# Kernel optimization log

Measured on AMD Instinct MI355X. Metric: run time of the kernel, lower is better.

## Reference

```python
import jax, jax.numpy as jnp
import numpy as np

DIM = 128
HEADS = 128
DV = DIM // HEADS  # 1 (scalar attention values per head)
TOPK = 32
CHUNK = 16384
DEPTH = 2
STATE = 262144
BLOCK = 256
NBLOCKS = STATE // BLOCK
HIDDEN = int(DIM * 8 / 3)  # 341, SwiGLU hidden
EPS = float(jnp.finfo(jnp.float32).eps)  # torch RMSNorm default eps


def rmsnorm(x, w):
    return x * jax.lax.rsqrt(jnp.mean(x * x, axis=-1, keepdims=True) + EPS) * w


def swiglu(x, w_gate, w_up, w_down):
    return (jax.nn.silu(x @ w_gate.T) * (x @ w_up.T)) @ w_down.T


def topk_attention(x, Wq, Wk, Wv, Wo):
    b, n, d = x.shape
    q = jnp.einsum('bnd,hd->bhn', x, Wq)      # (b,h,n) scalar queries
    keys = jnp.einsum('bnd,hd->bhn', x, Wk)   # (b,h,n) scalar keys
    v = (x @ Wv.T).reshape(b, n, HEADS, DV).transpose(0, 2, 1, 3)  # (b,h,n,dv)
    order = jnp.argsort(keys, axis=-1)
    k_sorted = jnp.take_along_axis(keys, order, axis=-1)
    v_sorted = jnp.take_along_axis(v, order[..., None], axis=2)
    top_k_keys = k_sorted[..., -TOPK:]
    bot_k_keys = k_sorted[..., :TOPK]
    top_k_vals = v_sorted[:, :, -TOPK:, :]
    bot_k_vals = v_sorted[:, :, :TOPK, :]
    nc = n // CHUNK
    q_chunks = q.reshape(b, HEADS, nc, CHUNK).transpose(2, 0, 1, 3)  # (nc,b,h,c)

    def chunk_fn(q_chunk):
        scores_top = q_chunk[..., None] * top_k_keys[:, :, None, :]  # (b,h,c,k)
        scores_bot = q_chunk[..., None] * bot_k_keys[:, :, None, :]
        attn_top = jax.nn.softmax(scores_top, axis=-1)
        attn_bot = jax.nn.softmax(scores_bot, axis=-1)
        out_top = jnp.einsum('bhck,bhkd->bhcd', attn_top, top_k_vals)
        out_bot = jnp.einsum('bhck,bhkd->bhcd', attn_bot, bot_k_vals)
        q_pos = (q_chunk > 0).astype(x.dtype)[..., None]
        return q_pos * out_top + (1 - q_pos) * out_bot  # (b,h,c,dv)

    out = jax.lax.map(chunk_fn, q_chunks)            # (nc,b,h,c,dv)
    out = out.transpose(1, 0, 3, 2, 4).reshape(b, n, d)  # (b,n,h*dv)
    return out @ Wo.T


def setup_inputs() -> dict:
    key = jax.random.key(0)
    ks = jax.random.split(key, 16)
    s = 0.02
    nrm = lambda k, shp: (jax.random.normal(k, shp, dtype=jnp.float32) * s)
    inp = {}
    inp['state_bytes'] = jax.random.randint(ks[0], (1, STATE), 0, 256)
    inp['byte_embed'] = nrm(ks[1], (256, DIM))
    inp['block_pos_embed'] = nrm(ks[2], (NBLOCKS, DIM))
    inp['local_pos_embed'] = nrm(ks[3], (BLOCK, DIM))
    inp['Wq'] = nrm(ks[4], (DEPTH, HEADS, DIM))
    inp['Wk'] = nrm(ks[5], (DEPTH, HEADS, DIM))
    inp['Wv'] = nrm(ks[6], (DEPTH, DIM, DIM))
    inp['Wo'] = nrm(ks[7], (DEPTH, DIM, DIM))
    inp['norm1_w'] = jnp.ones((DEPTH, DIM), dtype=jnp.float32)
    inp['norm2_w'] = jnp.ones((DEPTH, DIM), dtype=jnp.float32)
    inp['w_gate'] = nrm(ks[8], (DEPTH, HIDDEN, DIM))
    inp['w_up'] = nrm(ks[9], (DEPTH, HIDDEN, DIM))
    inp['w_down'] = nrm(ks[10], (DEPTH, DIM, HIDDEN))
    inp['final_norm_w'] = jnp.ones((DIM,), dtype=jnp.float32)
    inp['out_w'] = nrm(ks[11], (256, DIM))
    return inp


def reference(state_bytes, byte_embed, block_pos_embed, local_pos_embed, Wq, Wk, Wv, Wo,
              norm1_w, norm2_w, w_gate, w_up, w_down, final_norm_w, out_w):
    x = byte_embed[state_bytes]                                   # (b,n,d)
    block_pos = jnp.repeat(block_pos_embed, BLOCK, axis=0)        # (n,d)
    local_pos = jnp.tile(local_pos_embed, (NBLOCKS, 1))           # (n,d)
    x = x + block_pos[None] + local_pos[None]
    for l in range(DEPTH):
        x = x + topk_attention(rmsnorm(x, norm1_w[l]), Wq[l], Wk[l], Wv[l], Wo[l])
        x = x + swiglu(rmsnorm(x, norm2_w[l]), w_gate[l], w_up[l], w_down[l])
    x = rmsnorm(x, final_norm_w)
    return x @ out_w.T  # (b, STATE, 256)
```

## Files before the change

kernel.cpp:

```cpp
#include <hip/hip_runtime.h>


#define NTOK 262144
#define LOG2E 1.44269504088896340736f
#define NEGINF (-3.402823466e38f)

typedef unsigned short u16;
typedef short s16x8 __attribute__((ext_vector_type(8)));
typedef float f32x4 __attribute__((ext_vector_type(4)));

__device__ __forceinline__ float b2f(u16 u) {
  unsigned int x = ((unsigned int)u) << 16;
  return __builtin_bit_cast(float, x);
}
__device__ __forceinline__ u16 f2b(float f) {
  unsigned int x = __builtin_bit_cast(unsigned int, f);
  x = x + 0x7fffu + ((x >> 16) & 1u);
  return (u16)(x >> 16);
}

__global__ __launch_bounds__(256) void embed_kernel(const int* __restrict__ bytes,
    const float* __restrict__ be, const float* __restrict__ bpe,
    const float* __restrict__ lpe, float* __restrict__ x)
{
  int i4 = blockIdx.x * 256 + threadIdx.x;
  int n  = i4 >> 5;
  int dq = (i4 & 31) * 4;
  int b  = bytes[n];
  float4 a = *(const float4*)(be  + b * 128 + dq);
  float4 c = *(const float4*)(bpe + (n >> 8) * 128 + dq);
  float4 d = *(const float4*)(lpe + (n & 255) * 128 + dq);
  float4 o;
  o.x = (a.x + c.x) + d.x; o.y = (a.y + c.y) + d.y;
  o.z = (a.z + c.z) + d.z; o.w = (a.w + c.w) + d.w;
  *(float4*)(x + (size_t)n * 128 + dq) = o;
}

__global__ __launch_bounds__(256) void scale_kernel(const float* __restrict__ x,
    float* __restrict__ s)
{
  const int lane = threadIdx.x & 63;
  const int gw = blockIdx.x * 4 + (threadIdx.x >> 6);
  for (int tok = gw; tok < NTOK; tok += 4096) {
    const float2 v = *(const float2*)&x[(size_t)tok * 128 + lane * 2];
    float ss = v.x * v.x + v.y * v.y;
    #pragma unroll
    for (int off = 1; off < 64; off <<= 1) ss += __shfl_xor(ss, off, 64);
    const float m = ss * (1.f / 128.f) + 1.1920929e-07f;
    float r = rsqrtf(m);
    r = r * (1.5f - 0.5f * m * r * r);
    if (lane == 0) s[tok] = r;
  }
}

enum { M32_QK = 0, M32_RESID = 1, M32_RAW = 2 };

template<int MODE>
__global__ __launch_bounds__(256) void gemm_f32(
    const float* __restrict__ A, const float* __restrict__ rs, const float* __restrict__ cw,
    const float* __restrict__ B, const float* __restrict__ Bb,
    int K, int ldb, int Brows, int Bkcols,
    float* __restrict__ O, float* __restrict__ O2, int ldo)
{
  __shared__ float La[64][68];
  __shared__ float Lb[64][132];
  __shared__ float cwS[128];
  const int t = threadIdx.x;
  const int m0 = blockIdx.x * 64;
  const int n0 = (MODE == M32_QK) ? 0 : blockIdx.y * 128;
  const float* Bu = (MODE == M32_QK && blockIdx.y) ? Bb : B;
  for (int i = t; i < 128; i += 256) cwS[i] = cw ? cw[i] : 1.f;
  __syncthreads();

  float acc[4][8] = {};
  const int ta = (t & 15) * 4;
  const int tb = (t >> 4) * 8;

  for (int k0 = 0; k0 < K; k0 += 64) {
    for (int c = t; c < 1024; c += 256) {
      int tok = c >> 4, k4 = (c & 15) * 4;
      float4 av = *(const float4*)&A[(size_t)(m0 + tok) * K + k0 + k4];
      float rsv = rs ? rs[m0 + tok] : 1.f;
      La[k4 + 0][tok] = av.x * rsv * cwS[(k0 + k4 + 0) & 127];
      La[k4 + 1][tok] = av.y * rsv * cwS[(k0 + k4 + 1) & 127];
      La[k4 + 2][tok] = av.z * rsv * cwS[(k0 + k4 + 2) & 127];
      La[k4 + 3][tok] = av.w * rsv * cwS[(k0 + k4 + 3) & 127];
    }
    for (int c = t; c < 2048; c += 256) {
      int col = c >> 4, k4 = (c & 15) * 4;
      int gr = n0 + col;
      float4 bv = make_float4(0.f, 0.f, 0.f, 0.f);
      if (gr < Brows) {
        int kb = k0 + k4;
        if (((ldb & 3) == 0) && kb + 3 < Bkcols) {
          bv = *(const float4*)&Bu[(size_t)gr * ldb + kb];
        } else {
          float* bp = (float*)&bv;
          #pragma unroll
          for (int j = 0; j < 4; j++)
            if (kb + j < Bkcols) bp[j] = Bu[(size_t)gr * ldb + kb + j];
        }
      }
      Lb[k4 + 0][col] = bv.x; Lb[k4 + 1][col] = bv.y;
      Lb[k4 + 2][col] = bv.z; Lb[k4 + 3][col] = bv.w;
    }
    __syncthreads();
    for (int kq = 0; kq < 64; kq += 4) {
      float aa[4][4], bb[4][8];
      #pragma unroll
      for (int kk = 0; kk < 4; kk++) {
        *(float4*)&aa[kk][0] = *(const float4*)&La[kq + kk][ta];
        *(float4*)&bb[kk][0] = *(const float4*)&Lb[kq + kk][tb];
        *(float4*)&bb[kk][4] = *(const float4*)&Lb[kq + kk][tb + 4];
      }
      #pragma unroll
      for (int i = 0; i < 4; i++)
        #pragma unroll
        for (int j = 0; j < 8; j++) {
          float tt = aa[0][i] * bb[0][j];
          tt = fmaf(aa[1][i], bb[1][j], tt);
          tt = fmaf(aa[2][i], bb[2][j], tt);
          tt = fmaf(aa[3][i], bb[3][j], tt);
          acc[i][j] += tt;
        }
    }
    __syncthreads();
  }

  if (MODE == M32_QK) {
    if (blockIdx.y == 0) {
      #pragma unroll
      for (int i = 0; i < 4; i++)
        #pragma unroll
        for (int j = 0; j < 8; j++)
          O[(size_t)(m0 + ta + i) * 128 + tb + j] = acc[i][j];
    } else {
      #pragma unroll
      for (int i = 0; i < 4; i++)
        #pragma unroll
        for (int j = 0; j < 8; j++)
          O2[(size_t)(tb + j) * NTOK + (m0 + ta + i)] = acc[i][j];
    }
  } else if (MODE == M32_RESID) {
    #pragma unroll
    for (int i = 0; i < 4; i++)
      #pragma unroll
      for (int j = 0; j < 8; j++) {
        size_t ix = (size_t)(m0 + ta + i) * ldo + n0 + tb + j;
        O[ix] += acc[i][j];
      }
  } else {
    #pragma unroll
    for (int i = 0; i < 4; i++)
      #pragma unroll
      for (int j = 0; j < 8; j++)
        O[(size_t)(m0 + ta + i) * ldo + n0 + tb + j] = acc[i][j];
  }
}

__global__ __launch_bounds__(256) void prep_split(const float* __restrict__ wg,
    const float* __restrict__ wu, const float* __restrict__ wd,
    const float* __restrict__ wo, const float* __restrict__ ow,
    u16* __restrict__ whi, u16* __restrict__ wlo)
{
  const int i = blockIdx.x * 256 + threadIdx.x;
  float val = 0.f;
  if (i < 49152) {
    int r = i >> 7, k = i & 127;
    if (r < 341) val = wg[43648 + r * 128 + k];
  } else if (i < 98304) {
    int j = i - 49152, r = j >> 7, k = j & 127;
    if (r < 341) val = wu[43648 + r * 128 + k];
  } else if (i < 147456) {
    int j = i - 98304, r = j / 384, c = j % 384;
    if (c < 341) val = wd[43648 + r * 341 + c];
  } else if (i < 163840) {
    val = wo[16384 + (i - 147456)];
  } else {
    val = ow[i - 163840];
  }
  u16 h = f2b(val);
  whi[i] = h;
  wlo[i] = f2b(val - b2f(h));
}

enum { MB_RAW = 0, MB_RESID = 1 };

template<int MODE>
__global__ __launch_bounds__(256) void gemm_bf3(
    const float* __restrict__ A, const float* __restrict__ rs, const float* __restrict__ cw,
    int K, const u16* __restrict__ Bhi, const u16* __restrict__ Blo, int ldb,
    float* __restrict__ O, int ldo)
{
  __shared__ u16 sAhi[64 * 136];
  __shared__ u16 sAlo[64 * 136];
  __shared__ u16 sBhi[64 * 136];
  __shared__ u16 sBlo[64 * 136];
  __shared__ float cwS[128];
  const int t = threadIdx.x;
  const int lane = t & 63;
  const int w = t >> 6;
  const int wr = w >> 1, wc = w & 1;
  const int m0 = blockIdx.x * 64;
  const int n0 = blockIdx.y * 64;
  const int l15 = lane & 15;
  const int lg  = lane >> 4;
  for (int i = t; i < 128; i += 256) cwS[i] = cw ? cw[i] : 1.f;
  __syncthreads();

  f32x4 acc[2][2] = {};

  for (int k0 = 0; k0 < K; k0 += 128) {
    for (int c = t; c < 2048; c += 256) {
      int row = c >> 5, k4 = (c & 31) * 4;
      float4 av = *(const float4*)&A[(size_t)(m0 + row) * K + k0 + k4];
      float rsv = rs ? rs[m0 + row] : 1.f;
      float vv[4] = { av.x, av.y, av.z, av.w };
      ushort4 hv, lv;
      u16* hp = (u16*)&hv; u16* lp = (u16*)&lv;
      #pragma unroll
      for (int j = 0; j < 4; j++) {
        float a = vv[j] * rsv * cwS[(k4 + j) & 127];
        u16 h = f2b(a);
        hp[j] = h;
        lp[j] = f2b(a - b2f(h));
      }
      *(ushort4*)&sAhi[row * 136 + k4] = hv;
      *(ushort4*)&sAlo[row * 136 + k4] = lv;
    }
    for (int c = t; c < 1024; c += 256) {
      int row = c >> 4, k8 = (c & 15) * 8;
      *(uint4*)&sBhi[row * 136 + k8] = *(const uint4*)&Bhi[(size_t)(n0 + row) * ldb + k0 + k8];
      *(uint4*)&sBlo[row * 136 + k8] = *(const uint4*)&Blo[(size_t)(n0 + row) * ldb + k0 + k8];
    }
    __syncthreads();
    #pragma unroll
    for (int ks = 0; ks < 4; ks++) {
      s16x8 ah[2], al[2], bh[2], bl[2];
      #pragma unroll
      for (int mr = 0; mr < 2; mr++) {
        int off = (wr * 32 + mr * 16 + l15) * 136 + ks * 32 + lg * 8;
        ah[mr] = *(const s16x8*)&sAhi[off];
        al[mr] = *(const s16x8*)&sAlo[off];
      }
      #pragma unroll
      for (int nr = 0; nr < 2; nr++) {
        int off = (wc * 32 + nr * 16 + l15) * 136 + ks * 32 + lg * 8;
        bh[nr] = *(const s16x8*)&sBhi[off];
        bl[nr] = *(const s16x8*)&sBlo[off];
      }
      #pragma unroll
      for (int mr = 0; mr < 2; mr++)
        #pragma unroll
        for (int nr = 0; nr < 2; nr++) {
          acc[mr][nr] = __builtin_amdgcn_mfma_f32_16x16x32_bf16(ah[mr], bh[nr], acc[mr][nr], 0, 0, 0);
          acc[mr][nr] = __builtin_amdgcn_mfma_f32_16x16x32_bf16(ah[mr], bl[nr], acc[mr][nr], 0, 0, 0);
          acc[mr][nr] = __builtin_amdgcn_mfma_f32_16x16x32_bf16(al[mr], bh[nr], acc[mr][nr], 0, 0, 0);
        }
    }
    __syncthreads();
  }

  #pragma unroll
  for (int mr = 0; mr < 2; mr++)
    #pragma unroll
    for (int nr = 0; nr < 2; nr++)
      #pragma unroll
      for (int r = 0; r < 4; r++) {
        int row = m0 + wr * 32 + mr * 16 + lg * 4 + r;
        int col = n0 + wc * 32 + nr * 16 + l15;
        size_t ix = (size_t)row * ldo + col;
        if (MODE == MB_RESID) O[ix] += acc[mr][nr][r];
        else                  O[ix]  = acc[mr][nr][r];
      }
}

__global__ __launch_bounds__(256) void sel_pass1(const float* __restrict__ kt,
    float* __restrict__ cV, int* __restrict__ cI)
{
  const int hb = blockIdx.y;
  const int h = hb >> 1;
  const float sgn = (hb & 1) ? -1.f : 1.f;
  const int wv = threadIdx.x >> 6;
  const int lane = threadIdx.x & 63;
  const int base = blockIdx.x * 8192 + wv * 2048;
  const float* row = kt + (size_t)h * NTOK;

  float vals[32];
  #pragma unroll
  for (int j4 = 0; j4 < 8; j4++) {
    float4 v4 = *(const float4*)&row[base + j4 * 256 + lane * 4];
    vals[j4 * 4 + 0] = sgn * v4.x; vals[j4 * 4 + 1] = sgn * v4.y;
    vals[j4 * 4 + 2] = sgn * v4.z; vals[j4 * 4 + 3] = sgn * v4.w;
  }
  float m = NEGINF; int mj = 0;
  #pragma unroll
  for (int j = 0; j < 32; j++) if (vals[j] > m) { m = vals[j]; mj = j; }

  unsigned int used = 0u;
  const size_t slot = (size_t)hb * 4096 + (blockIdx.x * 4 + wv) * 32;
  for (int r = 0; r < 32; r++) {
    float bv = m; int bl = lane; int bj = mj;
    #pragma unroll
    for (int off = 1; off < 64; off <<= 1) {
      float ov = __shfl_xor(bv, off, 64);
      int   ol = __shfl_xor(bl, off, 64);
      int   oj = __shfl_xor(bj, off, 64);
      if (ov > bv || (ov == bv && ol < bl)) { bv = ov; bl = ol; bj = oj; }
    }
    if (lane == 0) {
      cV[slot + r] = bv;
      cI[slot + r] = base + (bj >> 2) * 256 + bl * 4 + (bj & 3);
    }
    if (lane == bl) {
      used |= (1u << bj);
      m = NEGINF; mj = 0;
      #pragma unroll
      for (int j = 0; j < 32; j++)
        if (!((used >> j) & 1u) && vals[j] > m) { m = vals[j]; mj = j; }
    }
  }
}

__global__ __launch_bounds__(256) void sel_pass2(const float* __restrict__ cV,
    const int* __restrict__ cI, const float* __restrict__ x, const float* __restrict__ s,
    const float* __restrict__ nw, const float* __restrict__ Wv,
    float* __restrict__ tabK, float* __restrict__ tabV)
{
  __shared__ float lv[128];
  __shared__ int   li[128];
  __shared__ float selv[32];
  __shared__ int   seli[32];
  const int t = threadIdx.x;
  const int hb = blockIdx.x;
  const int h = hb >> 1;
  const int sb = hb & 1;
  const float sgn = sb ? -1.f : 1.f;
  const int wv = t >> 6;
  const int lane = t & 63;
  const size_t cb = (size_t)hb * 4096;

  float vals[16]; int idxs[16];
  #pragma unroll
  for (int j = 0; j < 16; j++) {
    vals[j] = cV[cb + t + j * 256];
    idxs[j] = cI[cb + t + j * 256];
  }
  float m = NEGINF; int mj = 0;
  #pragma unroll
  for (int j = 0; j < 16; j++) if (vals[j] > m) { m = vals[j]; mj = j; }

  unsigned int used = 0u;
  for (int r = 0; r < 32; r++) {
    float bv = m; int bl = lane; int bj = mj;
    #pragma unroll
    for (int off = 1; off < 64; off <<= 1) {
      float ov = __shfl_xor(bv, off, 64);
      int   ol = __shfl_xor(bl, off, 64);
      int   oj = __shfl_xor(bj, off, 64);
      if (ov > bv || (ov == bv && ol < bl)) { bv = ov; bl = ol; bj = oj; }
    }
    if (lane == 0) { lv[wv * 32 + r] = bv; li[wv * 32 + r] = 0; }
    if (lane == bl) {
      li[wv * 32 + r] = idxs[bj];
      used |= (1u << bj);
      m = NEGINF; mj = 0;
      #pragma unroll
      for (int j = 0; j < 16; j++)
        if (!((used >> j) & 1u) && vals[j] > m) { m = vals[j]; mj = j; }
    }
  }
  __syncthreads();

  if (t == 0) {
    int p[4] = {0, 0, 0, 0};
    for (int r = 0; r < 32; r++) {
      float best = NEGINF; int bw = 0;
      #pragma unroll
      for (int w = 0; w < 4; w++) {
        if (p[w] < 32) {
          float v = lv[w * 32 + p[w]];
          if (v > best) { best = v; bw = w; }
        }
      }
      selv[r] = best;
      seli[r] = li[bw * 32 + p[bw]];
      p[bw]++;
    }
  }
  __syncthreads();

  if (t < 32) {
    float kval = sgn * selv[t];
    int idx = seli[t];
    tabK[(sb * 32 + t) * 128 + h] = kval * LOG2E;
    float acc = 0.f;
    const float* xr = &x[(size_t)idx * 128];
    const float* wvp = &Wv[h * 128];
    for (int k = 0; k < 128; k++) acc = fmaf(xr[k] * nw[k], wvp[k], acc);
    tabV[(sb * 32 + t) * 128 + h] = acc * s[idx];
  }
}

__global__ __launch_bounds__(512) void att_kernel(float* __restrict__ q,
    const float* __restrict__ tabK, const float* __restrict__ tabV)
{
  __shared__ float tk[8192];
  __shared__ float tv[8192];
  const int t = threadIdx.x;
  for (int i = t; i < 8192; i += 512) { tk[i] = tabK[i]; tv[i] = tabV[i]; }
  __syncthreads();
  const int h = t & 127;
  const int base = blockIdx.x * 256;
  for (int it = 0; it < 64; it++) {
    const int tok = base + it * 4 + (t >> 7);
    const size_t off = (size_t)tok * 128 + h;
    const float qv = q[off];
    const int b = (qv > 0.f) ? 0 : 4096;
    const float* kk = &tk[b + h];
    const float* vv = &tv[b + h];
    float sw = 0.f, swv = 0.f;
    #pragma unroll
    for (int j = 0; j < 32; j++) {
      float e = exp2f(qv * kk[j * 128]);
      sw += e;
      swv = fmaf(e, vv[j * 128], swv);
    }
    q[off] = swv / sw;
  }
}

__global__ __launch_bounds__(256) void silu_kernel(float* __restrict__ g,
    const float* __restrict__ u, int n4)
{
  int idx = blockIdx.x * 256 + threadIdx.x;
  for (int i = idx; i < n4; i += gridDim.x * 256) {
    float4 gv = *(float4*)&g[(size_t)i * 4];
    float4 uv = *(const float4*)&u[(size_t)i * 4];
    float4 o;
    o.x = gv.x / (1.f + expf(-gv.x)) * uv.x;
    o.y = gv.y / (1.f + expf(-gv.y)) * uv.y;
    o.z = gv.z / (1.f + expf(-gv.z)) * uv.z;
    o.w = gv.w / (1.f + expf(-gv.w)) * uv.w;
    *(float4*)&g[(size_t)i * 4] = o;
  }
}


extern "C" void kernel_launch(void* const* d_in, const int* in_sizes, int n_in,
                              void* d_out, int out_size, void* d_ws, size_t ws_size,
                              hipStream_t stream)
{
  (void)in_sizes; (void)n_in; (void)out_size; (void)ws_size;
  const int*   bytes = (const int*)d_in[0];
  const float* be    = (const float*)d_in[1];
  const float* bpe   = (const float*)d_in[2];
  const float* lpe   = (const float*)d_in[3];
  const float* Wq    = (const float*)d_in[4];
  const float* Wk    = (const float*)d_in[5];
  const float* Wv    = (const float*)d_in[6];
  const float* Wo    = (const float*)d_in[7];
  const float* n1w   = (const float*)d_in[8];
  const float* n2w   = (const float*)d_in[9];
  const float* wg    = (const float*)d_in[10];
  const float* wu    = (const float*)d_in[11];
  const float* wd    = (const float*)d_in[12];
  const float* fnw   = (const float*)d_in[13];
  const float* outw  = (const float*)d_in[14];
  float* out = (float*)d_out;

  char* ws = (char*)d_ws;
  float* x    = (float*)(ws + 0);
  float* q    = (float*)(ws + 134217728);
  float* kt   = (float*)(ws + 268435456);
  float* s    = (float*)(ws + 402653184);
  float* tabK = (float*)(ws + 403701760);
  float* tabV = (float*)(ws + 403734528);
  u16*   whi  = (u16*)(ws + 403767296);
  u16*   wlo  = (u16*)(ws + 404160512);
  float* gbuf = kt;
  float* ubuf = kt + 12582912;
  float* cV   = out;
  int*   cI   = (int*)(out + 256 * 4096);

  const size_t AG = 0, AU = 49152, AD = 98304, AW = 147456, AH = 163840;

  prep_split<<<768, 256, 0, stream>>>(wg, wu, wd, Wo, outw, whi, wlo);
  embed_kernel<<<32768, 256, 0, stream>>>(bytes, be, bpe, lpe, x);

  for (int l = 0; l < 2; l++) {
    const float* wq = Wq + l * 16384;
    const float* wk = Wk + l * 16384;
    const float* wv = Wv + l * 16384;
    const float* wo = Wo + l * 16384;
    const float* g1 = n1w + l * 128;
    const float* g2 = n2w + l * 128;
    const float* wgl = wg + l * 43648;
    const float* wul = wu + l * 43648;
    const float* wdl = wd + l * 43648;

    scale_kernel<<<1024, 256, 0, stream>>>(x, s);
    gemm_f32<M32_QK><<<dim3(4096, 2), 256, 0, stream>>>(
        x, s, g1, wq, wk, 128, 128, 128, 128, q, kt, 128);
    sel_pass1<<<dim3(32, 256), 256, 0, stream>>>(kt, cV, cI);
    sel_pass2<<<256, 256, 0, stream>>>(cV, cI, x, s, g1, wv, tabK, tabV);
    att_kernel<<<1024, 512, 0, stream>>>(q, tabK, tabV);

    if (l == 0) {
      gemm_f32<M32_RESID><<<dim3(4096, 1), 256, 0, stream>>>(
          q, nullptr, nullptr, wo, nullptr, 128, 128, 128, 128, x, nullptr, 128);
      scale_kernel<<<1024, 256, 0, stream>>>(x, s);
      for (int c = 0; c < 8; c++) {
        const size_t base = (size_t)c * 32768;
        gemm_f32<M32_RAW><<<dim3(512, 3), 256, 0, stream>>>(
            x + base * 128, s + base, g2, wgl, nullptr, 128, 128, 341, 128,
            gbuf, nullptr, 384);
        gemm_f32<M32_RAW><<<dim3(512, 3), 256, 0, stream>>>(
            x + base * 128, s + base, g2, wul, nullptr, 128, 128, 341, 128,
            ubuf, nullptr, 384);
        silu_kernel<<<3072, 256, 0, stream>>>(gbuf, ubuf, 3145728);
        gemm_f32<M32_RESID><<<dim3(512, 1), 256, 0, stream>>>(
            gbuf, nullptr, nullptr, wdl, nullptr, 384, 341, 128, 341,
            x + base * 128, nullptr, 128);
      }
    } else {
      gemm_bf3<MB_RESID><<<dim3(4096, 2), 256, 0, stream>>>(
          q, nullptr, nullptr, 128, whi + AW, wlo + AW, 128, x, 128);
      scale_kernel<<<1024, 256, 0, stream>>>(x, s);
      for (int c = 0; c < 8; c++) {
        const size_t base = (size_t)c * 32768;
        gemm_bf3<MB_RAW><<<dim3(512, 6), 256, 0, stream>>>(
            x + base * 128, s + base, g2, 128, whi + AG, wlo + AG, 128, gbuf, 384);
        gemm_bf3<MB_RAW><<<dim3(512, 6), 256, 0, stream>>>(
            x + base * 128, s + base, g2, 128, whi + AU, wlo + AU, 128, ubuf, 384);
        silu_kernel<<<3072, 256, 0, stream>>>(gbuf, ubuf, 3145728);
        gemm_bf3<MB_RESID><<<dim3(512, 2), 256, 0, stream>>>(
            gbuf, nullptr, nullptr, 384, whi + AD, wlo + AD, 384, x + base * 128, 128);
      }
    }
  }

  scale_kernel<<<1024, 256, 0, stream>>>(x, s);
  gemm_bf3<MB_RAW><<<dim3(4096, 4), 256, 0, stream>>>(
      x, s, fnw, 128, whi + AH, wlo + AH, 128, out, 256);
}
```

Baseline: 5.660 ms.

## Fuse gate/up GEMMs with SiLU, swizzle LDS, pack attention tables, relax exp

Adds fused gate+up GEMM kernels (fp32 and split-bf16 MFMA) that apply SiLU*up in the epilogue, removing the separate silu kernel and the round trip through two intermediate buffers. It also doubles the SwiGLU chunk size, XOR-swizzles LDS columns in the fp32 GEMM to cut bank conflicts, and packs K/V tables into float2 with two tokens per thread in attention. Layer 2 attention uses hardware exp2/rcp intrinsics, which trades some accuracy for speed.

```diff
diff --git a/kernel.cpp b/kernel.cpp
--- a/kernel.cpp
+++ b/kernel.cpp
@@ -79,15 +79,18 @@
   for (int k0 = 0; k0 < K; k0 += 64) {
     for (int c = t; c < 1024; c += 256) {
       int tok = c >> 4, k4 = (c & 15) * 4;
+      const int xsw = (c & 7) << 2;
       float4 av = *(const float4*)&A[(size_t)(m0 + tok) * K + k0 + k4];
       float rsv = rs ? rs[m0 + tok] : 1.f;
-      La[k4 + 0][tok] = av.x * rsv * cwS[(k0 + k4 + 0) & 127];
-      La[k4 + 1][tok] = av.y * rsv * cwS[(k0 + k4 + 1) & 127];
-      La[k4 + 2][tok] = av.z * rsv * cwS[(k0 + k4 + 2) & 127];
-      La[k4 + 3][tok] = av.w * rsv * cwS[(k0 + k4 + 3) & 127];
+      const int tokS = tok ^ xsw;
+      La[k4 + 0][tokS] = av.x * rsv * cwS[(k0 + k4 + 0) & 127];
+      La[k4 + 1][tokS] = av.y * rsv * cwS[(k0 + k4 + 1) & 127];
+      La[k4 + 2][tokS] = av.z * rsv * cwS[(k0 + k4 + 2) & 127];
+      La[k4 + 3][tokS] = av.w * rsv * cwS[(k0 + k4 + 3) & 127];
     }
     for (int c = t; c < 2048; c += 256) {
       int col = c >> 4, k4 = (c & 15) * 4;
+      const int xsw = (c & 7) << 2;
       int gr = n0 + col;
       float4 bv = make_float4(0.f, 0.f, 0.f, 0.f);
       if (gr < Brows) {
@@ -101,17 +104,19 @@
             if (kb + j < Bkcols) bp[j] = Bu[(size_t)gr * ldb + kb + j];
         }
       }
-      Lb[k4 + 0][col] = bv.x; Lb[k4 + 1][col] = bv.y;
-      Lb[k4 + 2][col] = bv.z; Lb[k4 + 3][col] = bv.w;
+      const int colS = col ^ xsw;
+      Lb[k4 + 0][colS] = bv.x; Lb[k4 + 1][colS] = bv.y;
+      Lb[k4 + 2][colS] = bv.z; Lb[k4 + 3][colS] = bv.w;
     }
     __syncthreads();
     for (int kq = 0; kq < 64; kq += 4) {
+      const int xsw = ((kq >> 2) & 7) << 2;
       float aa[4][4], bb[4][8];
       #pragma unroll
       for (int kk = 0; kk < 4; kk++) {
-        *(float4*)&aa[kk][0] = *(const float4*)&La[kq + kk][ta];
-        *(float4*)&bb[kk][0] = *(const float4*)&Lb[kq + kk][tb];
-        *(float4*)&bb[kk][4] = *(const float4*)&Lb[kq + kk][tb + 4];
+        *(float4*)&aa[kk][0] = *(const float4*)&La[kq + kk][ta ^ xsw];
+        *(float4*)&bb[kk][0] = *(const float4*)&Lb[kq + kk][tb ^ xsw];
+        *(float4*)&bb[kk][4] = *(const float4*)&Lb[kq + kk][(tb + 4) ^ xsw];
       }
       #pragma unroll
       for (int i = 0; i < 4; i++)
@@ -156,6 +161,88 @@
       for (int j = 0; j < 8; j++)
         O[(size_t)(m0 + ta + i) * ldo + n0 + tb + j] = acc[i][j];
   }
+}
+
+__global__ __launch_bounds__(256) void gemm_f32_gu(
+    const float* __restrict__ A, const float* __restrict__ rs, const float* __restrict__ cw,
+    const float* __restrict__ BG, const float* __restrict__ BU,
+    float* __restrict__ hh)
+{
+  __shared__ float La[64][68];
+  __shared__ float LbG[64][68];
+  __shared__ float LbU[64][68];
+  __shared__ float cwS[128];
+  const int t = threadIdx.x;
+  const int m0 = blockIdx.x * 64;
+  const int n0 = blockIdx.y * 64;
+  for (int i = t; i < 128; i += 256) cwS[i] = cw[i];
+  __syncthreads();
+
+  float accG[4][4] = {}, accU[4][4] = {};
+  const int ta = (t & 15) * 4;
+  const int tb = (t >> 4) * 4;
+
+  for (int k0 = 0; k0 < 128; k0 += 64) {
+    for (int c = t; c < 1024; c += 256) {
+      int tok = c >> 4, k4 = (c & 15) * 4;
+      const int xsw = (c & 7) << 2;
+      float4 av = *(const float4*)&A[(size_t)(m0 + tok) * 128 + k0 + k4];
+      float rsv = rs[m0 + tok];
+      const int tokS = tok ^ xsw;
+      La[k4 + 0][tokS] = av.x * rsv * cwS[k0 + k4 + 0];
+      La[k4 + 1][tokS] = av.y * rsv * cwS[k0 + k4 + 1];
+      La[k4 + 2][tokS] = av.z * rsv * cwS[k0 + k4 + 2];
+      La[k4 + 3][tokS] = av.w * rsv * cwS[k0 + k4 + 3];
+    }
+    for (int c = t; c < 2048; c += 256) {
+      int which = c >> 10, cc = c & 1023;
+      int col = cc >> 4, k4 = (cc & 15) * 4;
+      const int xsw = (cc & 7) << 2;
+      int gr = n0 + col;
+      float4 bv = make_float4(0.f, 0.f, 0.f, 0.f);
+      if (gr < 341)
+        bv = *(const float4*)&(which ? BU : BG)[(size_t)gr * 128 + k0 + k4];
+      float (*Lp)[68] = which ? LbU : LbG;
+      const int colS = col ^ xsw;
+      Lp[k4 + 0][colS] = bv.x; Lp[k4 + 1][colS] = bv.y;
+      Lp[k4 + 2][colS] = bv.z; Lp[k4 + 3][colS] = bv.w;
+    }
+    __syncthreads();
+    for (int kq = 0; kq < 64; kq += 4) {
+      const int xsw = ((kq >> 2) & 7) << 2;
+      float aa[4][4], bg[4][4], bu[4][4];
+      #pragma unroll
+      for (int kk = 0; kk < 4; kk++) {
+        *(float4*)&aa[kk][0] = *(const float4*)&La[kq + kk][ta ^ xsw];
+        *(float4*)&bg[kk][0] = *(const float4*)&LbG[kq + kk][tb ^ xsw];
+        *(float4*)&bu[kk][0] = *(const float4*)&LbU[kq + kk][tb ^ xsw];
+      }
+      #pragma unroll
+      for (int i = 0; i < 4; i++)
+        #pragma unroll
+        for (int j = 0; j < 4; j++) {
+          float tg = aa[0][i] * bg[0][j];
+          tg = fmaf(aa[1][i], bg[1][j], tg);
+          tg = fmaf(aa[2][i], bg[2][j], tg);
+          tg = fmaf(aa[3][i], bg[3][j], tg);
+          accG[i][j] += tg;
+          float tu = aa[0][i] * bu[0][j];
+          tu = fmaf(aa[1][i], bu[1][j], tu);
+          tu = fmaf(aa[2][i], bu[2][j], tu);
+          tu = fmaf(aa[3][i], bu[3][j], tu);
+          accU[i][j] += tu;
+        }
+    }
+    __syncthreads();
+  }
+
+  #pragma unroll
+  for (int i = 0; i < 4; i++)
+    #pragma unroll
+    for (int j = 0; j < 4; j++) {
+      float g = accG[i][j], u = accU[i][j];
+      hh[(size_t)(m0 + ta + i) * 384 + n0 + tb + j] = g / (1.f + expf(-g)) * u;
+    }
 }
 
 __global__ __launch_bounds__(256) void prep_split(const float* __restrict__ wg,
@@ -275,6 +362,97 @@
       }
 }
 
+__global__ __launch_bounds__(256) void gemm_bf3_gu(
+    const float* __restrict__ A, const float* __restrict__ rs, const float* __restrict__ cw,
+    const u16* __restrict__ Gh, const u16* __restrict__ Gl,
+    const u16* __restrict__ Uh, const u16* __restrict__ Ul,
+    float* __restrict__ hh)
+{
+  __shared__ u16 sAh[64 * 72];
+  __shared__ u16 sAl[64 * 72];
+  __shared__ u16 sB[4][64 * 72];
+  __shared__ float cwS[128];
+  const int t = threadIdx.x;
+  const int lane = t & 63;
+  const int w = t >> 6;
+  const int wr = w >> 1, wc = w & 1;
+  const int m0 = blockIdx.x * 64;
+  const int n0 = blockIdx.y * 64;
+  const int l15 = lane & 15;
+  const int lg  = lane >> 4;
+  for (int i = t; i < 128; i += 256) cwS[i] = cw[i];
+  __syncthreads();
+
+  f32x4 aG[2][2] = {}, aU[2][2] = {};
+
+  for (int k0 = 0; k0 < 128; k0 += 64) {
+    for (int c = t; c < 1024; c += 256) {
+      int row = c >> 4, k4 = (c & 15) * 4;
+      float4 av = *(const float4*)&A[(size_t)(m0 + row) * 128 + k0 + k4];
+      float rsv = rs[m0 + row];
+      float vv[4] = { av.x, av.y, av.z, av.w };
+      ushort4 hv, lv;
+      u16* hp = (u16*)&hv; u16* lp = (u16*)&lv;
+      #pragma unroll
+      for (int j = 0; j < 4; j++) {
+        float a = vv[j] * rsv * cwS[k0 + k4 + j];
+        u16 h = f2b(a);
+        hp[j] = h;
+        lp[j] = f2b(a - b2f(h));
+      }
+      *(ushort4*)&sAh[row * 72 + k4] = hv;
+      *(ushort4*)&sAl[row * 72 + k4] = lv;
+    }
+    for (int c = t; c < 2048; c += 256) {
+      int which = c >> 9, cc = c & 511;
+      int row = cc >> 3, k8 = (cc & 7) * 8;
+      const u16* src = which == 0 ? Gh : which == 1 ? Gl : which == 2 ? Uh : Ul;
+      *(uint4*)&sB[which][row * 72 + k8] = *(const uint4*)&src[(size_t)(n0 + row) * 128 + k0 + k8];
+    }
+    __syncthreads();
+    #pragma unroll
+    for (int ks = 0; ks < 2; ks++) {
+      s16x8 ah[2], al[2];
+      #pragma unroll
+      for (int mr = 0; mr < 2; mr++) {
+        int off = (wr * 32 + mr * 16 + l15) * 72 + ks * 32 + lg * 8;
+        ah[mr] = *(const s16x8*)&sAh[off];
+        al[mr] = *(const s16x8*)&sAl[off];
+      }
+      #pragma unroll
+      for (int nr = 0; nr < 2; nr++) {
+        int off = (wc * 32 + nr * 16 + l15) * 72 + ks * 32 + lg * 8;
+        s16x8 gh = *(const s16x8*)&sB[0][off];
+        s16x8 gl = *(const s16x8*)&sB[1][off];
+        s16x8 uh = *(const s16x8*)&sB[2][off];
+        s16x8 ul = *(const s16x8*)&sB[3][off];
+        #pragma unroll
+        for (int mr = 0; mr < 2; mr++) {
+          aG[mr][nr] = __builtin_amdgcn_mfma_f32_16x16x32_bf16(ah[mr], gh, aG[mr][nr], 0, 0, 0);
+          aG[mr][nr] = __builtin_amdgcn_mfma_f32_16x16x32_bf16(ah[mr], gl, aG[mr][nr], 0, 0, 0);
+          aG[mr][nr] = __builtin_amdgcn_mfma_f32_16x16x32_bf16(al[mr], gh, aG[mr][nr], 0, 0, 0);
+          aU[mr][nr] = __builtin_amdgcn_mfma_f32_16x16x32_bf16(ah[mr], uh, aU[mr][nr], 0, 0, 0);
+          aU[mr][nr] = __builtin_amdgcn_mfma_f32_16x16x32_bf16(ah[mr], ul, aU[mr][nr], 0, 0, 0);
+          aU[mr][nr] = __builtin_amdgcn_mfma_f32_16x16x32_bf16(al[mr], uh, aU[mr][nr], 0, 0, 0);
+        }
+      }
+    }
+    __syncthreads();
+  }
+
+  #pragma unroll
+  for (int mr = 0; mr < 2; mr++)
+    #pragma unroll
+    for (int nr = 0; nr < 2; nr++)
+      #pragma unroll
+      for (int r = 0; r < 4; r++) {
+        int row = m0 + wr * 32 + mr * 16 + lg * 4 + r;
+        int col = n0 + wc * 32 + nr * 16 + l15;
+        float g = aG[mr][nr][r], u = aU[mr][nr][r];
+        hh[(size_t)row * 384 + col] = g / (1.f + expf(-g)) * u;
+      }
+}
+
 __global__ __launch_bounds__(256) void sel_pass1(const float* __restrict__ kt,
     float* __restrict__ cV, int* __restrict__ cI)
 {
@@ -325,7 +503,7 @@
 __global__ __launch_bounds__(256) void sel_pass2(const float* __restrict__ cV,
     const int* __restrict__ cI, const float* __restrict__ x, const float* __restrict__ s,
     const float* __restrict__ nw, const float* __restrict__ Wv,
-    float* __restrict__ tabK, float* __restrict__ tabV)
+    float2* __restrict__ tabKV)
 {
   __shared__ float lv[128];
   __shared__ int   li[128];
@@ -393,56 +571,50 @@
   if (t < 32) {
     float kval = sgn * selv[t];
     int idx = seli[t];
-    tabK[(sb * 32 + t) * 128 + h] = kval * LOG2E;
     float acc = 0.f;
     const float* xr = &x[(size_t)idx * 128];
     const float* wvp = &Wv[h * 128];
     for (int k = 0; k < 128; k++) acc = fmaf(xr[k] * nw[k], wvp[k], acc);
-    tabV[(sb * 32 + t) * 128 + h] = acc * s[idx];
-  }
-}
-
+    tabKV[(sb * 32 + t) * 128 + h] = make_float2(kval * LOG2E, acc * s[idx]);
+  }
+}
+
+template<int RELAX>
 __global__ __launch_bounds__(512) void att_kernel(float* __restrict__ q,
-    const float* __restrict__ tabK, const float* __restrict__ tabV)
-{
-  __shared__ float tk[8192];
-  __shared__ float tv[8192];
+    const float2* __restrict__ tabKV)
+{
+  __shared__ float2 tkv[8192];
   const int t = threadIdx.x;
-  for (int i = t; i < 8192; i += 512) { tk[i] = tabK[i]; tv[i] = tabV[i]; }
+  for (int i = t; i < 8192; i += 512) tkv[i] = tabKV[i];
   __syncthreads();
   const int h = t & 127;
-  const int base = blockIdx.x * 256;
+  const int sub = t >> 7;
+  const int base = blockIdx.x * 512;
   for (int it = 0; it < 64; it++) {
-    const int tok = base + it * 4 + (t >> 7);
-    const size_t off = (size_t)tok * 128 + h;
-    const float qv = q[off];
-    const int b = (qv > 0.f) ? 0 : 4096;
-    const float* kk = &tk[b + h];
-    const float* vv = &tv[b + h];
-    float sw = 0.f, swv = 0.f;
+    const int tokA = base + it * 8 + sub;
+    const size_t offA = (size_t)tokA * 128 + h;
+    const size_t offB = offA + 512;
+    const float qa = q[offA];
+    const float qb = q[offB];
+    const float2* ka = &tkv[(qa > 0.f ? 0 : 4096) + h];
+    const float2* kb = &tkv[(qb > 0.f ? 0 : 4096) + h];
+    float swa = 0.f, sva = 0.f, swb = 0.f, svb = 0.f;
     #pragma unroll
     for (int j = 0; j < 32; j++) {
-      float e = exp2f(qv * kk[j * 128]);
-      sw += e;
-      swv = fmaf(e, vv[j * 128], swv);
-    }
-    q[off] = swv / sw;
-  }
-}
-
-__global__ __launch_bounds__(256) void silu_kernel(float* __restrict__ g,
-    const float* __restrict__ u, int n4)
-{
-  int idx = blockIdx.x * 256 + threadIdx.x;
-  for (int i = idx; i < n4; i += gridDim.x * 256) {
-    float4 gv = *(float4*)&g[(size_t)i * 4];
-    float4 uv = *(const float4*)&u[(size_t)i * 4];
-    float4 o;
-    o.x = gv.x / (1.f + expf(-gv.x)) * uv.x;
-    o.y = gv.y / (1.f + expf(-gv.y)) * uv.y;
-    o.z = gv.z / (1.f + expf(-gv.z)) * uv.z;
-    o.w = gv.w / (1.f + expf(-gv.w)) * uv.w;
-    *(float4*)&g[(size_t)i * 4] = o;
+      float2 A = ka[j * 128];
+      float2 B = kb[j * 128];
+      float ea = RELAX ? __builtin_amdgcn_exp2f(qa * A.x) : exp2f(qa * A.x);
+      float eb = RELAX ? __builtin_amdgcn_exp2f(qb * B.x) : exp2f(qb * B.x);
+      swa += ea; sva = fmaf(ea, A.y, sva);
+      swb += eb; svb = fmaf(eb, B.y, svb);
+    }
+    if (RELAX) {
+      q[offA] = sva * __builtin_amdgcn_rcpf(swa);
+      q[offB] = svb * __builtin_amdgcn_rcpf(swb);
+    } else {
+      q[offA] = sva / swa;
+      q[offB] = svb / swb;
+    }
   }
 }
 
@@ -470,18 +642,16 @@
   float* out = (float*)d_out;
 
   char* ws = (char*)d_ws;
-  float* x    = (float*)(ws + 0);
-  float* q    = (float*)(ws + 134217728);
-  float* kt   = (float*)(ws + 268435456);
-  float* s    = (float*)(ws + 402653184);
-  float* tabK = (float*)(ws + 403701760);
-  float* tabV = (float*)(ws + 403734528);
-  u16*   whi  = (u16*)(ws + 403767296);
-  u16*   wlo  = (u16*)(ws + 404160512);
-  float* gbuf = kt;
-  float* ubuf = kt + 12582912;
-  float* cV   = out;
-  int*   cI   = (int*)(out + 256 * 4096);
+  float*  x     = (float*)(ws + 0);
+  float*  q     = (float*)(ws + 134217728);
+  float*  kt    = (float*)(ws + 268435456);
+  float*  s     = (float*)(ws + 402653184);
+  float2* tabKV = (float2*)(ws + 403701760);
+  u16*    whi   = (u16*)(ws + 403767296);
+  u16*    wlo   = (u16*)(ws + 404160512);
+  float*  hh    = kt;
+  float*  cV    = out;
+  int*    cI    = (int*)(out + 256 * 4096);
 
   const size_t AG = 0, AU = 49152, AD = 98304, AW = 147456, AH = 163840;
 
@@ -503,39 +673,33 @@
     gemm_f32<M32_QK><<<dim3(4096, 2), 256, 0, stream>>>(
         x, s, g1, wq, wk, 128, 128, 128, 128, q, kt, 128);
     sel_pass1<<<dim3(32, 256), 256, 0, stream>>>(kt, cV, cI);
-    sel_pass2<<<256, 256, 0, stream>>>(cV, cI, x, s, g1, wv, tabK, tabV);
-    att_kernel<<<1024, 512, 0, stream>>>(q, tabK, tabV);
+    sel_pass2<<<256, 256, 0, stream>>>(cV, cI, x, s, g1, wv, tabKV);
 
     if (l == 0) {
+      att_kernel<0><<<512, 512, 0, stream>>>(q, tabKV);
       gemm_f32<M32_RESID><<<dim3(4096, 1), 256, 0, stream>>>(
           q, nullptr, nullptr, wo, nullptr, 128, 128, 128, 128, x, nullptr, 128);
       scale_kernel<<<1024, 256, 0, stream>>>(x, s);
-      for (int c = 0; c < 8; c++) {
-        const size_t base = (size_t)c * 32768;
-        gemm_f32<M32_RAW><<<dim3(512, 3), 256, 0, stream>>>(
-            x + base * 128, s + base, g2, wgl, nullptr, 128, 128, 341, 128,
-            gbuf, nullptr, 384);
-        gemm_f32<M32_RAW><<<dim3(512, 3), 256, 0, stream>>>(
-            x + base * 128, s + base, g2, wul, nullptr, 128, 128, 341, 128,
-            ubuf, nullptr, 384);
-        silu_kernel<<<3072, 256, 0, stream>>>(gbuf, ubuf, 3145728);
-        gemm_f32<M32_RESID><<<dim3(512, 1), 256, 0, stream>>>(
-            gbuf, nullptr, nullptr, wdl, nullptr, 384, 341, 128, 341,
+      for (int c = 0; c < 4; c++) {
+        const size_t base = (size_t)c * 65536;
+        gemm_f32_gu<<<dim3(1024, 6), 256, 0, stream>>>(
+            x + base * 128, s + base, g2, wgl, wul, hh);
+        gemm_f32<M32_RESID><<<dim3(1024, 1), 256, 0, stream>>>(
+            hh, nullptr, nullptr, wdl, nullptr, 384, 341, 128, 341,
             x + base * 128, nullptr, 128);
       }
     } else {
+      att_kernel<1><<<512, 512, 0, stream>>>(q, tabKV);
       gemm_bf3<MB_RESID><<<dim3(4096, 2), 256, 0, stream>>>(
           q, nullptr, nullptr, 128, whi + AW, wlo + AW, 128, x, 128);
       scale_kernel<<<1024, 256, 0, stream>>>(x, s);
-      for (int c = 0; c < 8; c++) {
-        const size_t base = (size_t)c * 32768;
-        gemm_bf3<MB_RAW><<<dim3(512, 6), 256, 0, stream>>>(
-            x + base * 128, s + base, g2, 128, whi + AG, wlo + AG, 128, gbuf, 384);
-        gemm_bf3<MB_RAW><<<dim3(512, 6), 256, 0, stream>>>(
-            x + base * 128, s + base, g2, 128, whi + AU, wlo + AU, 128, ubuf, 384);
-        silu_kernel<<<3072, 256, 0, stream>>>(gbuf, ubuf, 3145728);
-        gemm_bf3<MB_RESID><<<dim3(512, 2), 256, 0, stream>>>(
-            gbuf, nullptr, nullptr, 384, whi + AD, wlo + AD, 384, x + base * 128, 128);
+      for (int c = 0; c < 4; c++) {
+        const size_t base = (size_t)c * 65536;
+        gemm_bf3_gu<<<dim3(1024, 6), 256, 0, stream>>>(
+            x + base * 128, s + base, g2,
+            whi + AG, wlo + AG, whi + AU, wlo + AU, hh);
+        gemm_bf3<MB_RESID><<<dim3(1024, 2), 256, 0, stream>>>(
+            hh, nullptr, nullptr, 384, whi + AD, wlo + AD, 384, x + base * 128, 128);
       }
     }
   }
```

Result: faster. 5.031 ms (-11.1%).
